# Optimization experiments

Hardware: AMD Instinct MI355X
Metric: run time of the kernel (lower is better)

## Reference

```python
import jax, jax.numpy as jnp
import numpy as np

V, E, H, L = 32000, 256, 512, 2
B, T, S = 64, 64, 64


def setup_inputs() -> dict:
    key = jax.random.key(0)
    ks = jax.random.split(key, 20)
    p = lambda k, shape: (0.02 * jax.random.normal(k, shape)).astype(jnp.float32)
    return {
        "X": jax.random.randint(ks[0], (B, T), 0, V),
        "enc_outputs": jax.random.normal(ks[1], (B, S, H), dtype=jnp.float32),
        "hidden_state": jax.random.normal(ks[2], (L, B, H), dtype=jnp.float32),
        "enc_valid_lens": jax.random.randint(ks[3], (B,), 1, S + 1),
        "emb": p(ks[4], (V, E)),
        "Wq": p(ks[5], (H, H)),
        "Wk": p(ks[6], (H, H)),
        "wv": p(ks[7], (H,)),
        "W_ih0": p(ks[8], (3 * H, E + H)),
        "W_hh0": p(ks[9], (3 * H, H)),
        "b_ih0": p(ks[10], (3 * H,)),
        "b_hh0": p(ks[11], (3 * H,)),
        "W_ih1": p(ks[12], (3 * H, H)),
        "W_hh1": p(ks[13], (3 * H, H)),
        "b_ih1": p(ks[14], (3 * H,)),
        "b_hh1": p(ks[15], (3 * H,)),
        "dense_W": p(ks[16], (V, H)),
        "dense_b": p(ks[17], (V,)),
    }


def _gru_cell(x, h, W_ih, W_hh, b_ih, b_hh):
    gi = x @ W_ih.T + b_ih            # [B, 3H]
    gh = h @ W_hh.T + b_hh            # [B, 3H]
    i_r, i_z, i_n = jnp.split(gi, 3, axis=-1)
    h_r, h_z, h_n = jnp.split(gh, 3, axis=-1)
    r = jax.nn.sigmoid(i_r + h_r)
    z = jax.nn.sigmoid(i_z + h_z)
    n = jnp.tanh(i_n + r * h_n)
    return (1.0 - z) * n + z * h


def reference(X, enc_outputs, hidden_state, enc_valid_lens, emb, Wq, Wk, wv,
              W_ih0, W_hh0, b_ih0, b_hh0, W_ih1, W_hh1, b_ih1, b_hh1,
              dense_W, dense_b):
    # token embeddings, time-major: [T, B, E]
    x_seq = jnp.transpose(emb[X], (1, 0, 2))
    keys_proj = jnp.einsum('bsh,kh->bsk', enc_outputs, Wk)  # precompute W_k(K)
    valid_mask = jnp.arange(S)[None, :] < enc_valid_lens[:, None]  # [B, S]

    def step(h, x_t):
        q = h[-1] @ Wq.T                                     # [B, H]
        feat = jnp.tanh(q[:, None, :] + keys_proj)           # [B, S, H]
        scores = feat @ wv                                   # [B, S]
        attn = jax.nn.softmax(jnp.where(valid_mask, scores, -1e6), axis=-1)
        context = jnp.einsum('bs,bsh->bh', attn, enc_outputs)
        inp = jnp.concatenate([context, x_t], axis=-1)       # [B, H+E]
        h0 = _gru_cell(inp, h[0], W_ih0, W_hh0, b_ih0, b_hh0)
        h1 = _gru_cell(h0, h[1], W_ih1, W_hh1, b_ih1, b_hh1)
        return jnp.stack([h0, h1]), h1

    h_final, outs = jax.lax.scan(step, hidden_state, x_seq)  # outs: [T, B, H]
    logits = outs @ dense_W.T + dense_b                      # [T, B, V]
    return jnp.transpose(logits, (1, 0, 2))                  # [B, T, V]
```

## Files before the change

### kernel.cpp

```cpp
#include <hip/hip_runtime.h>
#include <hip/hip_bf16.h>
#include <hip/hip_fp16.h>

#define VV 32000
#define EE 256
#define HH 512
#define BB 64
#define TT 64
#define SS 64
#define G3 1536
#define NGRU 256
#define STU 16384

typedef __attribute__((ext_vector_type(8))) short bf16x8;
typedef __attribute__((ext_vector_type(4))) float f32x4;
typedef _Float16 half2v __attribute__((ext_vector_type(2)));

__device__ __forceinline__ half2v bch(unsigned u) { return __builtin_bit_cast(half2v, u); }

__device__ __forceinline__ void async16(void* lds, const void* g) {
  __builtin_amdgcn_global_load_lds((const __attribute__((address_space(1))) void*)g,
                                   (__attribute__((address_space(3))) void*)lds, 16, 0, 0);
}

__device__ __forceinline__ float sigmoid_fast(float x) {
  return 1.0f / (1.0f + __expf(-x));
}
__device__ __forceinline__ float tanh_fast(float x) {
  x = fminf(fmaxf(x, -15.f), 15.f);
  float e = __expf(2.f * x);
  return (e - 1.f) / (e + 1.f);
}
__device__ __forceinline__ float2 unpackh2(unsigned u) {
  __half2 h = *reinterpret_cast<__half2*>(&u);
  return __half22float2(h);
}
__device__ __forceinline__ unsigned packh2(float x, float y) {
  __half2 h = __floats2half2_rn(x, y);
  return *reinterpret_cast<unsigned*>(&h);
}
__device__ __forceinline__ unsigned packh2w(float x, float y) {
  half2v h; h[0] = (_Float16)x; h[1] = (_Float16)y;
  return __builtin_bit_cast(unsigned, h);
}

__device__ __forceinline__ void stg_sc(float* p, float v) {
  asm volatile("global_store_dword %0, %1, off sc0 sc1" :: "v"(p), "v"(v) : "memory");
}
__device__ __forceinline__ void stg_scu(unsigned* p, unsigned v) {
  asm volatile("global_store_dword %0, %1, off sc0 sc1" :: "v"(p), "v"(v) : "memory");
}
__device__ __forceinline__ void stg_scu2(unsigned* p, uint2 v) {
  asm volatile("global_store_dwordx2 %0, %1, off sc0 sc1" :: "v"(p), "v"(v) : "memory");
}
__device__ __forceinline__ void stg_sci(int* p, int v) {
  asm volatile("global_store_dword %0, %1, off sc0 sc1" :: "v"(p), "v"(v) : "memory");
}
__device__ __forceinline__ int ld_agent(const int* p) {
  return __hip_atomic_load(p, __ATOMIC_RELAXED, __HIP_MEMORY_SCOPE_AGENT);
}

template <int NBK>
__device__ __forceinline__ void gbar(int* flags, int* go, int phase) {
  __syncthreads();
  if (blockIdx.x == NBK - 1) {
    if (threadIdx.x < 64) {
      const int l = threadIdx.x;
      if (l == 0) stg_sci(&flags[NBK - 1], phase);
      for (;;) {
        bool ok = true;
#pragma unroll
        for (int g = 0; g < NBK / 64; ++g) ok &= (ld_agent(&flags[l + 64 * g]) >= phase);
        if (__all(ok)) break;
        __builtin_amdgcn_s_sleep(1);
      }
      if (l == 0) stg_sci(go, phase);
    }
  } else {
    if (threadIdx.x == 0) {
      stg_sci(&flags[blockIdx.x], phase);
      while (ld_agent(go) < phase) __builtin_amdgcn_s_sleep(1);
    }
  }
  __syncthreads();
}

__global__ __launch_bounds__(256) void transpose_kernel(float* __restrict__ dst,
                                                        const float* __restrict__ src,
                                                        int R, int C, int ld, int off) {
  __shared__ float tile[32][33];
  int c0 = blockIdx.x * 32, r0 = blockIdx.y * 32;
  int x = threadIdx.x, y = threadIdx.y;
  for (int i = y; i < 32; i += 8) tile[i][x] = src[(size_t)(r0 + i) * ld + off + c0 + x];
  __syncthreads();
  for (int i = y; i < 32; i += 8) dst[(size_t)(c0 + i) * R + r0 + x] = tile[x][i];
}

__global__ __launch_bounds__(256) void cast_kernel(const float* __restrict__ src,
                                                   __hip_bfloat16* __restrict__ dst, int n) {
  for (int i = blockIdx.x * blockDim.x + threadIdx.x; i < n; i += gridDim.x * blockDim.x)
    dst[i] = __float2bfloat16(src[i]);
}

__global__ __launch_bounds__(256) void packhalf_kernel(const float* __restrict__ src,
                                                       unsigned* __restrict__ dst, int npairs) {
  for (int i = blockIdx.x * blockDim.x + threadIdx.x; i < npairs; i += gridDim.x * blockDim.x)
    dst[i] = packh2(src[2 * i], src[2 * i + 1]);
}

__global__ __launch_bounds__(256) void hspack_kernel(const float* __restrict__ hs,
                                                     unsigned* __restrict__ h0u,
                                                     unsigned* __restrict__ h1u) {
  int i = blockIdx.x * 256 + threadIdx.x;
  int layer = i >> 14, r = i & 16383;
  int b = r >> 8, kp = r & 255;
  const float* src = hs + (size_t)layer * BB * HH + (size_t)b * HH + 2 * kp;
  unsigned u = packh2(src[0], src[1]);
  (layer ? h1u : h0u)[(kp >> 1) * 128 + 2 * b + (kp & 1)] = u;
}

__global__ __launch_bounds__(256) void gemm32_kernel(const float* __restrict__ A,
                                                     const int* __restrict__ Xtb,
                                                     const float* __restrict__ Bk,
                                                     const float* __restrict__ bias,
                                                     float* __restrict__ C,
                                                     int N, int K, int ldb, int tbmaj) {
  __shared__ float Xs[32][65];
  __shared__ float Ws[32][129];
  __shared__ int toks[64];
  int m0 = blockIdx.x * 64, n0 = blockIdx.y * 128;
  int tid = threadIdx.x;
  if (tid < 64) {
    int m = m0 + tid;
    toks[tid] = Xtb ? Xtb[(m & 63) * TT + (m >> 6)] : m;
  }
  __syncthreads();
  float acc[4][8];
#pragma unroll
  for (int i = 0; i < 4; ++i)
#pragma unroll
    for (int j = 0; j < 8; ++j) acc[i][j] = 0.f;
  int mi = (tid >> 4) * 4;
  int ni = (tid & 15) * 8;
  for (int kc = 0; kc < K; kc += 32) {
#pragma unroll
    for (int i = 0; i < 16; ++i) {
      int idx = tid + i * 256;
      int kk = idx >> 7, nn = idx & 127;
      Ws[kk][nn] = Bk[(size_t)(kc + kk) * ldb + n0 + nn];
    }
#pragma unroll
    for (int i = 0; i < 8; ++i) {
      int idx = tid + i * 256;
      int mm = idx >> 5, kk = idx & 31;
      Xs[kk][mm] = A[(size_t)toks[mm] * K + kc + kk];
    }
    __syncthreads();
#pragma unroll
    for (int k = 0; k < 32; ++k) {
      float xv[4], wv[8];
#pragma unroll
      for (int i = 0; i < 4; ++i) xv[i] = Xs[k][mi + i];
#pragma unroll
      for (int j = 0; j < 8; ++j) wv[j] = Ws[k][ni + j];
#pragma unroll
      for (int i = 0; i < 4; ++i)
#pragma unroll
        for (int j = 0; j < 8; ++j) acc[i][j] += xv[i] * wv[j];
    }
    __syncthreads();
  }
#pragma unroll
  for (int i = 0; i < 4; ++i) {
    int m = m0 + mi + i;
#pragma unroll
    for (int j = 0; j < 8; ++j) {
      int n = n0 + ni + j;
      float v = acc[i][j] + (bias ? bias[n] : 0.f);
      if (tbmaj) C[((size_t)(m >> 6) * N + n) * BB + (m & 63)] = v;
      else       C[(size_t)m * N + n] = v;
    }
  }
}

struct RecArgs {
  const float *Wq, *W_ih0, *W_hh0, *W_ih1, *W_hh1;
  const float *b_hh0, *b_ih1, *b_hh1;
  const float *gixT, *wv;
  const unsigned *keysph, *ench;
  const int* vlen;
  const unsigned *h0i, *h1i;
  float *qS;
  unsigned *ctxS, *h0S, *h1S;
  int *flags, *go;
  __hip_bfloat16* outsb;
};

__device__ __forceinline__ void accum6(const unsigned* __restrict__ xu, int xkp0,
                                       const unsigned (*__restrict__ WL)[8], int wkp0,
                                       int nkp, int b, float s[6]) {
#pragma unroll 4
  for (int i = 0; i < nkp; i += 2) {
    uint2 xv = *(const uint2*)(xu + ((xkp0 + i) >> 1) * 128 + 2 * b);
    half2v x0 = bch(xv.x), x1 = bch(xv.y);
    const unsigned* w0 = WL[wkp0 + i];
    const unsigned* w1 = WL[wkp0 + i + 1];
#pragma unroll
    for (int g = 0; g < 6; ++g) {
      s[g] = __builtin_amdgcn_fdot2(bch(w0[g]), x0, s[g], false);
      s[g] = __builtin_amdgcn_fdot2(bch(w1[g]), x1, s[g], false);
    }
  }
}

template <bool HOIST, int NBK>
__global__ __launch_bounds__(512, 4) void recurrent_kernel(RecArgs a) {
  const int blk = blockIdx.x, tid = threadIdx.x;
  const int w = tid >> 6, lane = tid & 63;
  const bool isGru = HOIST ? (blk < NGRU) : true;
  const bool isAttn = HOIST ? (blk >= NGRU) : (blk < BB);
  const int battn = HOIST ? (blk - NGRU) : blk;
  const int j0 = 2 * blk;

  __shared__ __align__(16) unsigned WLh[2][512][8];
  __shared__ __align__(16) unsigned QLh[256][2];
  __shared__ float redW[6][8][64];
  __shared__ float redH0s[6][64], redH1s[6][64];
  __shared__ float sQ[HH], sWV[HH], sCt[HH], sAttn[SS];

  if (isGru) {
    for (int idx = tid; idx < 2 * 3072; idx += 512) {
      int layer = idx / 3072;
      int rem = idx - layer * 3072;
      int kp = rem / 6, g = rem - kp * 6;
      int gate = g >> 1, jj = g & 1;
      int row = gate * 512 + j0 + jj;
      float w0, w1;
      if (layer == 0) {
        if (kp < 256) { w0 = a.W_ih0[(size_t)row * 768 + 2 * kp];
                        w1 = a.W_ih0[(size_t)row * 768 + 2 * kp + 1]; }
        else          { w0 = a.W_hh0[(size_t)row * 512 + 2 * (kp - 256)];
                        w1 = a.W_hh0[(size_t)row * 512 + 2 * (kp - 256) + 1]; }
      } else {
        if (kp < 256) { w0 = a.W_ih1[(size_t)row * 512 + 2 * kp];
                        w1 = a.W_ih1[(size_t)row * 512 + 2 * kp + 1]; }
        else          { w0 = a.W_hh1[(size_t)row * 512 + 2 * (kp - 256)];
                        w1 = a.W_hh1[(size_t)row * 512 + 2 * (kp - 256) + 1]; }
      }
      WLh[layer][kp][g] = packh2w(w0, w1);
    }
    {
      int kp = tid >> 1, jj = tid & 1;
      QLh[kp][jj] = packh2w(a.Wq[(size_t)(j0 + jj) * HH + 2 * kp],
                            a.Wq[(size_t)(j0 + jj) * HH + 2 * kp + 1]);
    }
  }
  if (isAttn) sWV[tid] = a.wv[tid];
  const int vl = isAttn ? a.vlen[battn] : 0;
  const int hoff = isGru ? ((blk >> 1) * 128 + (blk & 1)) : 0;
  __syncthreads();

  for (int t = 0; t < TT; ++t) {
    const unsigned* h0p = (t == 0) ? a.h0i : a.h0S + (size_t)(t - 1) * STU;
    const unsigned* h1p = (t == 0) ? a.h1i : a.h1S + (size_t)(t - 1) * STU;
    float* qrowT = a.qS + (size_t)t * BB * HH;
    unsigned* ctxu = a.ctxS + (size_t)t * STU;
    unsigned* h0n  = a.h0S + (size_t)t * STU;
    unsigned* h1n  = a.h1S + (size_t)t * STU;

    if (isGru) {
      float q0 = 0.f, q1 = 0.f;
      const int kp0 = w * 32;
#pragma unroll 4
      for (int i = 0; i < 32; i += 2) {
        uint2 xv = *(const uint2*)(h1p + ((kp0 + i) >> 1) * 128 + 2 * lane);
        half2v x0 = bch(xv.x), x1 = bch(xv.y);
        q0 = __builtin_amdgcn_fdot2(bch(QLh[kp0 + i][0]), x0, q0, false);
        q0 = __builtin_amdgcn_fdot2(bch(QLh[kp0 + i + 1][0]), x1, q0, false);
        q1 = __builtin_amdgcn_fdot2(bch(QLh[kp0 + i][1]), x0, q1, false);
        q1 = __builtin_amdgcn_fdot2(bch(QLh[kp0 + i + 1][1]), x1, q1, false);
      }
      redW[0][w][lane] = q0; redW[1][w][lane] = q1;
      __syncthreads();
      if (tid < 64) {
        int b = tid;
        float v0 = 0.f, v1 = 0.f;
#pragma unroll
        for (int q = 0; q < 8; ++q) { v0 += redW[0][q][b]; v1 += redW[1][q][b]; }
        stg_sc(&qrowT[(size_t)b * HH + j0], v0);
        stg_sc(&qrowT[(size_t)b * HH + j0 + 1], v1);
      }
    }
    gbar<NBK>(a.flags, a.go, t * 4 + 1);

    if (HOIST && isGru) {
      float s[6] = {0, 0, 0, 0, 0, 0};
      const int layer = (w >= 4) ? 1 : 0;
      const unsigned* xp = layer ? h1p : h0p;
      const int c = (w & 3) * 64;
      accum6(xp, c, WLh[layer], 256 + c, 64, lane, s);
#pragma unroll
      for (int g = 0; g < 6; ++g) redW[g][w][lane] = s[g];
      __syncthreads();
      if (tid < 128) {
        int b = tid & 63, jj = tid >> 6;
#pragma unroll
        for (int g = 0; g < 3; ++g) {
          int sl = 2 * g + jj;
          redH0s[sl][b] = redW[sl][0][b] + redW[sl][1][b] + redW[sl][2][b] + redW[sl][3][b];
          redH1s[sl][b] = redW[sl][4][b] + redW[sl][5][b] + redW[sl][6][b] + redW[sl][7][b];
        }
      }
    } else if (isAttn) {
      const int b = battn;
      sQ[tid] = qrowT[(size_t)b * HH + tid];
      __syncthreads();
      for (int s = w; s < SS; s += 8) {
        const unsigned* kp = a.keysph + ((size_t)b * SS + s) * 256;
        float p = 0.f;
#pragma unroll
        for (int i = 0; i < 4; ++i) {
          int hp = lane + 64 * i;
          float2 kv = unpackh2(kp[hp]);
          p += tanh_fast(sQ[2 * hp] + kv.x) * sWV[2 * hp]
             + tanh_fast(sQ[2 * hp + 1] + kv.y) * sWV[2 * hp + 1];
        }
#pragma unroll
        for (int off = 32; off > 0; off >>= 1) p += __shfl_down(p, off);
        if (lane == 0) sAttn[s] = (s < vl) ? p : -1e6f;
      }
      __syncthreads();
      if (w == 0) {
        float v = sAttn[lane];
        float mx = v;
        for (int off = 32; off > 0; off >>= 1) mx = fmaxf(mx, __shfl_xor(mx, off));
        float e = __expf(v - mx);
        float sm = e;
        for (int off = 32; off > 0; off >>= 1) sm += __shfl_xor(sm, off);
        sAttn[lane] = e / sm;
      }
      __syncthreads();
      if (tid < 256) {
        float c0 = 0.f, c1 = 0.f;
        const unsigned* ep = a.ench + (size_t)b * SS * 256 + tid;
#pragma unroll 8
        for (int s = 0; s < SS; ++s) {
          float at = sAttn[s];
          float2 ev = unpackh2(ep[s * 256]);
          c0 += at * ev.x; c1 += at * ev.y;
        }
        sCt[2 * tid] = c0; sCt[2 * tid + 1] = c1;
      }
      __syncthreads();
      if (tid < 128) {
        uint2 v;
        v.x = packh2(sCt[4 * tid], sCt[4 * tid + 1]);
        v.y = packh2(sCt[4 * tid + 2], sCt[4 * tid + 3]);
        stg_scu2(&ctxu[tid * 128 + 2 * b], v);
      }
    }
    gbar<NBK>(a.flags, a.go, t * 4 + 2);

    if (isGru) {
      float gr0, gz0, gn0, gr1, gz1, gn1;
      unsigned holdu = 0;
      if (tid < 64) {
        const int b = tid;
        const float* gx = a.gixT + (size_t)t * G3 * BB;
        gr0 = gx[(size_t)(j0)*BB + b];          gr1 = gx[(size_t)(j0 + 1) * BB + b];
        gz0 = gx[(size_t)(j0 + 512) * BB + b];  gz1 = gx[(size_t)(j0 + 513) * BB + b];
        gn0 = gx[(size_t)(j0 + 1024) * BB + b]; gn1 = gx[(size_t)(j0 + 1025) * BB + b];
        holdu = h0p[hoff + 2 * b];
      }
      float s[6] = {0, 0, 0, 0, 0, 0};
      if (HOIST) {
        accum6(ctxu, w * 32, WLh[0], w * 32, 32, lane, s);
      } else {
        const int c = (w & 3) * 64;
        if (w < 4) accum6(ctxu, c, WLh[0], c, 64, lane, s);
        else       accum6(h0p,  c, WLh[0], 256 + c, 64, lane, s);
      }
#pragma unroll
      for (int g = 0; g < 6; ++g) redW[g][w][lane] = s[g];
      __syncthreads();
      if (tid < 64) {
        const int b = tid;
        float2 hold = unpackh2(holdu);
        float hv[2];
#pragma unroll
        for (int jj = 0; jj < 2; ++jj) {
          int j = j0 + jj;
          float Ri = 0, Zi = 0, Ni = 0, Rh = 0, Zh = 0, Nh = 0;
          if (HOIST) {
#pragma unroll
            for (int q = 0; q < 8; ++q) {
              Ri += redW[jj][q][b]; Zi += redW[2 + jj][q][b]; Ni += redW[4 + jj][q][b];
            }
            Rh = redH0s[jj][b]; Zh = redH0s[2 + jj][b]; Nh = redH0s[4 + jj][b];
          } else {
#pragma unroll
            for (int q = 0; q < 4; ++q) {
              Ri += redW[jj][q][b];     Rh += redW[jj][4 + q][b];
              Zi += redW[2 + jj][q][b]; Zh += redW[2 + jj][4 + q][b];
              Ni += redW[4 + jj][q][b]; Nh += redW[4 + jj][4 + q][b];
            }
          }
          float gr = jj ? gr1 : gr0, gz = jj ? gz1 : gz0, gn = jj ? gn1 : gn0;
          float r = sigmoid_fast(gr + Ri + a.b_hh0[j] + Rh);
          float z = sigmoid_fast(gz + Zi + a.b_hh0[j + 512] + Zh);
          float n = tanh_fast(gn + Ni + r * (a.b_hh0[j + 1024] + Nh));
          float ho = jj ? hold.y : hold.x;
          hv[jj] = (1.f - z) * n + z * ho;
        }
        stg_scu(&h0n[hoff + 2 * b], packh2(hv[0], hv[1]));
      }
    }
    gbar<NBK>(a.flags, a.go, t * 4 + 3);

    if (isGru) {
      unsigned holdu = 0;
      if (tid < 64) holdu = h1p[hoff + 2 * tid];
      float s[6] = {0, 0, 0, 0, 0, 0};
      if (HOIST) {
        accum6(h0n, w * 32, WLh[1], w * 32, 32, lane, s);
      } else {
        const int c = (w & 3) * 64;
        if (w < 4) accum6(h0n, c, WLh[1], c, 64, lane, s);
        else       accum6(h1p, c, WLh[1], 256 + c, 64, lane, s);
      }
#pragma unroll
      for (int g = 0; g < 6; ++g) redW[g][w][lane] = s[g];
      __syncthreads();
      if (tid < 64) {
        const int b = tid;
        float2 hold = unpackh2(holdu);
        float hv[2];
#pragma unroll
        for (int jj = 0; jj < 2; ++jj) {
          int j = j0 + jj;
          float Ri = 0, Zi = 0, Ni = 0, Rh = 0, Zh = 0, Nh = 0;
          if (HOIST) {
#pragma unroll
            for (int q = 0; q < 8; ++q) {
              Ri += redW[jj][q][b]; Zi += redW[2 + jj][q][b]; Ni += redW[4 + jj][q][b];
            }
            Rh = redH1s[jj][b]; Zh = redH1s[2 + jj][b]; Nh = redH1s[4 + jj][b];
          } else {
#pragma unroll
            for (int q = 0; q < 4; ++q) {
              Ri += redW[jj][q][b];     Rh += redW[jj][4 + q][b];
              Zi += redW[2 + jj][q][b]; Zh += redW[2 + jj][4 + q][b];
              Ni += redW[4 + jj][q][b]; Nh += redW[4 + jj][4 + q][b];
            }
          }
          float r = sigmoid_fast(a.b_ih1[j] + Ri + a.b_hh1[j] + Rh);
          float z = sigmoid_fast(a.b_ih1[j + 512] + Zi + a.b_hh1[j + 512] + Zh);
          float n = tanh_fast(a.b_ih1[j + 1024] + Ni + r * (a.b_hh1[j + 1024] + Nh));
          float ho = jj ? hold.y : hold.x;
          hv[jj] = (1.f - z) * n + z * ho;
          a.outsb[((size_t)t * BB + b) * HH + j] = __float2bfloat16(hv[jj]);
        }
        stg_scu(&h1n[hoff + 2 * b], packh2(hv[0], hv[1]));
      }
    }
    gbar<NBK>(a.flags, a.go, t * 4 + 4);
  }
}

__global__ __launch_bounds__(256) void dense_kernel(const __hip_bfloat16* __restrict__ A,
                                                    const __hip_bfloat16* __restrict__ Bt,
                                                    const float* __restrict__ bias,
                                                    float* __restrict__ out) {
  __shared__ __align__(16) short As[128 * 64];
  __shared__ __align__(16) short Bs[128 * 64];
  int mt = blockIdx.x;
  int nt = blockIdx.y;
  int tid = threadIdx.x;
  int w = tid >> 6, lane = tid & 63;
  int wm = w >> 1, wn = w & 1;
  f32x4 acc[4][4];
#pragma unroll
  for (int m = 0; m < 4; ++m)
#pragma unroll
    for (int n = 0; n < 4; ++n) acc[m][n] = (f32x4)0.f;

  const short* Ag = (const short*)A + (size_t)(mt * 128) * 512;
  const short* Bg = (const short*)Bt + (size_t)(nt * 128) * 512;

  for (int kt = 0; kt < 8; ++kt) {
    int k0 = kt * 64;
#pragma unroll
    for (int c = 0; c < 4; ++c) {
      int chunk = w * 4 + c;
      int row = chunk * 8 + (lane >> 3);
      int col = (lane & 7) * 8;
      async16(As + chunk * 512, Ag + (size_t)row * 512 + k0 + col);
      async16(Bs + chunk * 512, Bg + (size_t)row * 512 + k0 + col);
    }
    __syncthreads();
#pragma unroll
    for (int kk = 0; kk < 2; ++kk) {
      int krow = kk * 32 + (lane >> 4) * 8;
      bf16x8 af[4], bf[4];
#pragma unroll
      for (int m = 0; m < 4; ++m) {
        int r = wm * 64 + m * 16 + (lane & 15);
        af[m] = *(const bf16x8*)&As[r * 64 + krow];
      }
#pragma unroll
      for (int n = 0; n < 4; ++n) {
        int r = wn * 64 + n * 16 + (lane & 15);
        bf[n] = *(const bf16x8*)&Bs[r * 64 + krow];
      }
#pragma unroll
      for (int m = 0; m < 4; ++m)
#pragma unroll
        for (int n = 0; n < 4; ++n)
          acc[m][n] = __builtin_amdgcn_mfma_f32_16x16x32_bf16(af[m], bf[n], acc[m][n], 0, 0, 0);
    }
    __syncthreads();
  }
#pragma unroll
  for (int m = 0; m < 4; ++m) {
    int rbase = mt * 128 + wm * 64 + m * 16 + (lane >> 4) * 4;
#pragma unroll
    for (int n = 0; n < 4; ++n) {
      int v = nt * 128 + wn * 64 + n * 16 + (lane & 15);
      float bv = bias[v];
#pragma unroll
      for (int r = 0; r < 4; ++r) {
        int mi = rbase + r;
        size_t off = (size_t)(mi & 63) * (TT * VV) + (size_t)(mi >> 6) * VV + v;
        out[off] = acc[m][n][r] + bv;
      }
    }
  }
}

extern "C" void kernel_launch(void* const* d_in, const int* in_sizes, int n_in,
                              void* d_out, int out_size, void* d_ws, size_t ws_size,
                              hipStream_t stream) {
  const int*   X     = (const int*)d_in[0];
  const float* enc   = (const float*)d_in[1];
  const float* hs    = (const float*)d_in[2];
  const int*   vlen  = (const int*)d_in[3];
  const float* emb   = (const float*)d_in[4];
  const float* Wq    = (const float*)d_in[5];
  const float* Wk    = (const float*)d_in[6];
  const float* wv    = (const float*)d_in[7];
  const float* W_ih0 = (const float*)d_in[8];
  const float* W_hh0 = (const float*)d_in[9];
  const float* b_ih0 = (const float*)d_in[10];
  const float* b_hh0 = (const float*)d_in[11];
  const float* W_ih1 = (const float*)d_in[12];
  const float* W_hh1 = (const float*)d_in[13];
  const float* b_ih1 = (const float*)d_in[14];
  const float* b_hh1 = (const float*)d_in[15];
  const float* dW    = (const float*)d_in[16];
  const float* db    = (const float*)d_in[17];
  float* out = (float*)d_out;

  char* wp = (char*)d_ws;
  auto alloc = [&](size_t bytes) { char* p = wp; wp += (bytes + 255) & ~(size_t)255; return p; };
  __hip_bfloat16* dWb   = (__hip_bfloat16*)alloc((size_t)VV * HH * 2);
  __hip_bfloat16* outsb = (__hip_bfloat16*)alloc((size_t)TT * BB * HH * 2);
  float* keysp = (float*)alloc((size_t)BB * SS * HH * 4);
  float* gixT  = (float*)alloc((size_t)TT * G3 * BB * 4);
  float* WkT   = (float*)alloc((size_t)HH * HH * 4);
  float* WT0e  = (float*)alloc((size_t)EE * G3 * 4);
  float* qS    = (float*)alloc((size_t)TT * BB * HH * 4);
  unsigned* keysph = (unsigned*)alloc((size_t)BB * SS * 256 * 4);
  unsigned* ench   = (unsigned*)alloc((size_t)BB * SS * 256 * 4);
  unsigned* h0i  = (unsigned*)alloc((size_t)STU * 4);
  unsigned* h1i  = (unsigned*)alloc((size_t)STU * 4);
  unsigned* ctxS = (unsigned*)alloc((size_t)TT * STU * 4);
  unsigned* h0S  = (unsigned*)alloc((size_t)TT * STU * 4);
  unsigned* h1S  = (unsigned*)alloc((size_t)TT * STU * 4);
  int* flags = (int*)alloc(320 * sizeof(int));
  int* go    = (int*)alloc(64 * sizeof(int));

  hipMemsetAsync(flags, 0, 320 * sizeof(int), stream);
  hipMemsetAsync(go, 0, 64 * sizeof(int), stream);

  dim3 tb(32, 8);
  transpose_kernel<<<dim3(HH / 32, HH / 32), tb, 0, stream>>>(WkT, Wk, HH, HH, HH, 0);
  transpose_kernel<<<dim3(EE / 32, G3 / 32), tb, 0, stream>>>(WT0e, W_ih0, G3, EE, HH + EE, HH);
  cast_kernel<<<2048, 256, 0, stream>>>(dW, dWb, VV * HH);
  hspack_kernel<<<128, 256, 0, stream>>>(hs, h0i, h1i);

  gemm32_kernel<<<dim3(BB * SS / 64, HH / 128), 256, 0, stream>>>(
      enc, nullptr, WkT, nullptr, keysp, HH, HH, HH, 0);
  gemm32_kernel<<<dim3(TT * BB / 64, G3 / 128), 256, 0, stream>>>(
      emb, X, WT0e, b_ih0, gixT, G3, EE, G3, 1);
  packhalf_kernel<<<1024, 256, 0, stream>>>(keysp, keysph, BB * SS * 256);
  packhalf_kernel<<<1024, 256, 0, stream>>>(enc, ench, BB * SS * 256);

  RecArgs args;
  args.Wq = Wq; args.W_ih0 = W_ih0; args.W_hh0 = W_hh0; args.W_ih1 = W_ih1; args.W_hh1 = W_hh1;
  args.b_hh0 = b_hh0; args.b_ih1 = b_ih1; args.b_hh1 = b_hh1;
  args.gixT = gixT; args.wv = wv; args.keysph = keysph; args.ench = ench; args.vlen = vlen;
  args.h0i = h0i; args.h1i = h1i;
  args.qS = qS; args.ctxS = ctxS; args.h0S = h0S; args.h1S = h1S;
  args.flags = flags; args.go = go; args.outsb = outsb;
  void* kp[] = {&args};

  int maxb = 0;
  hipError_t qe = hipOccupancyMaxActiveBlocksPerMultiprocessor(
      &maxb, reinterpret_cast<const void*>(recurrent_kernel<true, 320>), 512, 0);
  bool launchedA = false;
  if (qe == hipSuccess && maxb >= 2) {
    hipError_t le = hipLaunchCooperativeKernel(
        reinterpret_cast<void*>(recurrent_kernel<true, 320>),
        dim3(320), dim3(512), kp, 0, stream);
    launchedA = (le == hipSuccess);
  }
  if (!launchedA) {
    hipLaunchCooperativeKernel(
        reinterpret_cast<void*>(recurrent_kernel<false, 256>),
        dim3(256), dim3(512), kp, 0, stream);
  }

  dense_kernel<<<dim3(32, 250), 256, 0, stream>>>(outsb, dWb, db, out);
}
```

Measured before the change: 2.061 ms.

## Compute attention query inside attention blocks to drop a grid barrier per step

The query projection q = h1 @ Wq^T was previously split across GRU blocks, written to global memory, and followed by a grid-wide barrier before attention could read it. Now each attention block computes its own batch row's query directly from h1, using a pre-packed, transposed fp16 copy of Wq read from global memory. This removes one of four grid barriers per timestep and the qS round trip through memory. In exchange, each attention block does a 512x512 matvec per step with strided global reads of Wq, which adds work to the critical path of the attention phase.

```diff
diff --git a/kernel.cpp b/kernel.cpp
--- a/kernel.cpp
+++ b/kernel.cpp
@@ -44,9 +44,6 @@
   return __builtin_bit_cast(unsigned, h);
 }
 
-__device__ __forceinline__ void stg_sc(float* p, float v) {
-  asm volatile("global_store_dword %0, %1, off sc0 sc1" :: "v"(p), "v"(v) : "memory");
-}
 __device__ __forceinline__ void stg_scu(unsigned* p, unsigned v) {
   asm volatile("global_store_dword %0, %1, off sc0 sc1" :: "v"(p), "v"(v) : "memory");
 }
@@ -106,6 +103,20 @@
                                                        unsigned* __restrict__ dst, int npairs) {
   for (int i = blockIdx.x * blockDim.x + threadIdx.x; i < npairs; i += gridDim.x * blockDim.x)
     dst[i] = packh2(src[2 * i], src[2 * i + 1]);
+}
+
+__global__ __launch_bounds__(256) void packWqT_kernel(const float* __restrict__ Wq,
+                                                      unsigned* __restrict__ WqhT) {
+  __shared__ unsigned tile[32][33];
+  int kp0 = blockIdx.x * 32, j0 = blockIdx.y * 32;
+  int x = threadIdx.x, y = threadIdx.y;
+  for (int i = y; i < 32; i += 8) {
+    int j = j0 + i, kp = kp0 + x;
+    tile[i][x] = packh2(Wq[(size_t)j * HH + 2 * kp], Wq[(size_t)j * HH + 2 * kp + 1]);
+  }
+  __syncthreads();
+  for (int i = y; i < 32; i += 8)
+    WqhT[(size_t)(kp0 + i) * HH + j0 + x] = tile[x][i];
 }
 
 __global__ __launch_bounds__(256) void hspack_kernel(const float* __restrict__ hs,
@@ -184,13 +195,13 @@
 }
 
 struct RecArgs {
-  const float *Wq, *W_ih0, *W_hh0, *W_ih1, *W_hh1;
+  const float *W_ih0, *W_hh0, *W_ih1, *W_hh1;
   const float *b_hh0, *b_ih1, *b_hh1;
   const float *gixT, *wv;
+  const unsigned *WqhT;
   const unsigned *keysph, *ench;
   const int* vlen;
   const unsigned *h0i, *h1i;
-  float *qS;
   unsigned *ctxS, *h0S, *h1S;
   int *flags, *go;
   __hip_bfloat16* outsb;
@@ -223,9 +234,9 @@
   const int j0 = 2 * blk;
 
   __shared__ __align__(16) unsigned WLh[2][512][8];
-  __shared__ __align__(16) unsigned QLh[256][2];
   __shared__ float redW[6][8][64];
   __shared__ float redH0s[6][64], redH1s[6][64];
+  __shared__ unsigned sH2[256];
   __shared__ float sQ[HH], sWV[HH], sCt[HH], sAttn[SS];
 
   if (isGru) {
@@ -249,11 +260,6 @@
       }
       WLh[layer][kp][g] = packh2w(w0, w1);
     }
-    {
-      int kp = tid >> 1, jj = tid & 1;
-      QLh[kp][jj] = packh2w(a.Wq[(size_t)(j0 + jj) * HH + 2 * kp],
-                            a.Wq[(size_t)(j0 + jj) * HH + 2 * kp + 1]);
-    }
   }
   if (isAttn) sWV[tid] = a.wv[tid];
   const int vl = isAttn ? a.vlen[battn] : 0;
@@ -263,35 +269,9 @@
   for (int t = 0; t < TT; ++t) {
     const unsigned* h0p = (t == 0) ? a.h0i : a.h0S + (size_t)(t - 1) * STU;
     const unsigned* h1p = (t == 0) ? a.h1i : a.h1S + (size_t)(t - 1) * STU;
-    float* qrowT = a.qS + (size_t)t * BB * HH;
     unsigned* ctxu = a.ctxS + (size_t)t * STU;
     unsigned* h0n  = a.h0S + (size_t)t * STU;
     unsigned* h1n  = a.h1S + (size_t)t * STU;
-
-    if (isGru) {
-      float q0 = 0.f, q1 = 0.f;
-      const int kp0 = w * 32;
-#pragma unroll 4
-      for (int i = 0; i < 32; i += 2) {
-        uint2 xv = *(const uint2*)(h1p + ((kp0 + i) >> 1) * 128 + 2 * lane);
-        half2v x0 = bch(xv.x), x1 = bch(xv.y);
-        q0 = __builtin_amdgcn_fdot2(bch(QLh[kp0 + i][0]), x0, q0, false);
-        q0 = __builtin_amdgcn_fdot2(bch(QLh[kp0 + i + 1][0]), x1, q0, false);
-        q1 = __builtin_amdgcn_fdot2(bch(QLh[kp0 + i][1]), x0, q1, false);
-        q1 = __builtin_amdgcn_fdot2(bch(QLh[kp0 + i + 1][1]), x1, q1, false);
-      }
-      redW[0][w][lane] = q0; redW[1][w][lane] = q1;
-      __syncthreads();
-      if (tid < 64) {
-        int b = tid;
-        float v0 = 0.f, v1 = 0.f;
-#pragma unroll
-        for (int q = 0; q < 8; ++q) { v0 += redW[0][q][b]; v1 += redW[1][q][b]; }
-        stg_sc(&qrowT[(size_t)b * HH + j0], v0);
-        stg_sc(&qrowT[(size_t)b * HH + j0 + 1], v1);
-      }
-    }
-    gbar<NBK>(a.flags, a.go, t * 4 + 1);
 
     if (HOIST && isGru) {
       float s[6] = {0, 0, 0, 0, 0, 0};
@@ -313,7 +293,16 @@
       }
     } else if (isAttn) {
       const int b = battn;
-      sQ[tid] = qrowT[(size_t)b * HH + tid];
+      if (tid < 256) sH2[tid] = h1p[(tid >> 1) * 128 + 2 * b + (tid & 1)];
+      __syncthreads();
+      {
+        float q = 0.f;
+        const unsigned* wq = a.WqhT + tid;
+#pragma unroll 16
+        for (int kp = 0; kp < 256; ++kp)
+          q = __builtin_amdgcn_fdot2(bch(wq[(size_t)kp * HH]), bch(sH2[kp]), q, false);
+        sQ[tid] = q;
+      }
       __syncthreads();
       for (int s = w; s < SS; s += 8) {
         const unsigned* kp = a.keysph + ((size_t)b * SS + s) * 256;
@@ -359,7 +348,7 @@
         stg_scu2(&ctxu[tid * 128 + 2 * b], v);
       }
     }
-    gbar<NBK>(a.flags, a.go, t * 4 + 2);
+    gbar<NBK>(a.flags, a.go, t * 3 + 1);
 
     if (isGru) {
       float gr0, gz0, gn0, gr1, gz1, gn1;
@@ -415,7 +404,7 @@
         stg_scu(&h0n[hoff + 2 * b], packh2(hv[0], hv[1]));
       }
     }
-    gbar<NBK>(a.flags, a.go, t * 4 + 3);
+    gbar<NBK>(a.flags, a.go, t * 3 + 2);
 
     if (isGru) {
       unsigned holdu = 0;
@@ -463,7 +452,7 @@
         stg_scu(&h1n[hoff + 2 * b], packh2(hv[0], hv[1]));
       }
     }
-    gbar<NBK>(a.flags, a.go, t * 4 + 4);
+    gbar<NBK>(a.flags, a.go, t * 3 + 3);
   }
 }
 
@@ -568,7 +557,7 @@
   float* gixT  = (float*)alloc((size_t)TT * G3 * BB * 4);
   float* WkT   = (float*)alloc((size_t)HH * HH * 4);
   float* WT0e  = (float*)alloc((size_t)EE * G3 * 4);
-  float* qS    = (float*)alloc((size_t)TT * BB * HH * 4);
+  unsigned* WqhT   = (unsigned*)alloc((size_t)256 * HH * 4);
   unsigned* keysph = (unsigned*)alloc((size_t)BB * SS * 256 * 4);
   unsigned* ench   = (unsigned*)alloc((size_t)BB * SS * 256 * 4);
   unsigned* h0i  = (unsigned*)alloc((size_t)STU * 4);
@@ -587,6 +576,7 @@
   transpose_kernel<<<dim3(EE / 32, G3 / 32), tb, 0, stream>>>(WT0e, W_ih0, G3, EE, HH + EE, HH);
   cast_kernel<<<2048, 256, 0, stream>>>(dW, dWb, VV * HH);
   hspack_kernel<<<128, 256, 0, stream>>>(hs, h0i, h1i);
+  packWqT_kernel<<<dim3(256 / 32, HH / 32), tb, 0, stream>>>(Wq, WqhT);
 
   gemm32_kernel<<<dim3(BB * SS / 64, HH / 128), 256, 0, stream>>>(
       enc, nullptr, WkT, nullptr, keysp, HH, HH, HH, 0);
@@ -596,11 +586,12 @@
   packhalf_kernel<<<1024, 256, 0, stream>>>(enc, ench, BB * SS * 256);
 
   RecArgs args;
-  args.Wq = Wq; args.W_ih0 = W_ih0; args.W_hh0 = W_hh0; args.W_ih1 = W_ih1; args.W_hh1 = W_hh1;
+  args.W_ih0 = W_ih0; args.W_hh0 = W_hh0; args.W_ih1 = W_ih1; args.W_hh1 = W_hh1;
   args.b_hh0 = b_hh0; args.b_ih1 = b_ih1; args.b_hh1 = b_hh1;
-  args.gixT = gixT; args.wv = wv; args.keysph = keysph; args.ench = ench; args.vlen = vlen;
+  args.gixT = gixT; args.wv = wv; args.WqhT = WqhT;
+  args.keysph = keysph; args.ench = ench; args.vlen = vlen;
   args.h0i = h0i; args.h1i = h1i;
-  args.qS = qS; args.ctxS = ctxS; args.h0S = h0S; args.h1S = h1S;
+  args.ctxS = ctxS; args.h0S = h0S; args.h1S = h1S;
   args.flags = flags; args.go = go; args.outsb = outsb;
   void* kp[] = {&args};
 
```

New measurement: 2.262 ms. 1.1x slower.
